# Kernel optimization log

Hardware: AMD Instinct MI355X
Metric: run time of the kernel (lower is better)

The kernel has to match this reference:

```python
import jax, jax.numpy as jnp
import numpy as np

B, S, D = 2, 512, 256

def setup_inputs() -> dict:
    key = jax.random.key(0)
    k1, k2, k3, k4, k5 = jax.random.split(key, 5)
    return {
        "query": jax.random.normal(k1, (B, S, D), dtype=jnp.float32),
        "key": jax.random.normal(k2, (B, S, D), dtype=jnp.float32),
        "value": jax.random.normal(k3, (B, S, D), dtype=jnp.float32),
        "Wm_w": jax.random.normal(k4, (D, D), dtype=jnp.float32) * (1.0 / np.sqrt(D)),
        "vm_w": jax.random.normal(k5, (1, D), dtype=jnp.float32) * (1.0 / np.sqrt(D)),
    }

def reference(query, key, value, Wm_w, vm_w):
    # pairwise difference: q.unsqueeze(1) - q.unsqueeze(2) -> [B, S, S, D]
    diff = query[:, None, :, :] - query[:, :, None, :]
    # Wm (Linear, no bias): [B,S,S,D] @ Wm_w^T, then tanh
    h = jnp.tanh(jnp.einsum('bijd,ed->bije', diff, Wm_w))
    # vm (Linear D->1, no bias) + squeeze -> scores [B, S, S]
    sjt = jnp.einsum('bije,e->bij', h, vm_w[0])
    # softmax over dim=2 (eval mode: dropout is identity)
    atten = jax.nn.softmax(sjt, axis=2)
    # bmm(atten, value) -> [B, S, D]
    context = jnp.einsum('bij,bjd->bid', atten, value)
    return context, atten
```

## Files before the change

kernel.cpp:

```cpp
#include <hip/hip_runtime.h>

#define B 2
#define S 512
#define D 256
#define C2L 2.885390081777927f
#define LOG2E 1.4426950408889634f

__global__ __launch_bounds__(256) void proj_kernel(const float* __restrict__ q,
                                                   const float* __restrict__ W,
                                                   float* __restrict__ EJ,
                                                   float* __restrict__ EN) {
    __shared__ float qlds[4 * D];
    const int t = threadIdx.x;
    const int b = blockIdx.x / (S / 4);
    const int i0 = (blockIdx.x % (S / 4)) * 4;
    const float* qbase = q + (size_t)(b * S + i0) * D;
    for (int idx = t; idx < 4 * D; idx += 256) qlds[idx] = qbase[idx];
    __syncthreads();
    const float* wr = W + (size_t)t * D;
    float a0 = 0.f, a1 = 0.f, a2 = 0.f, a3 = 0.f;
#pragma unroll 4
    for (int d = 0; d < D; ++d) {
        float w = wr[d];
        a0 = fmaf(qlds[d], w, a0);
        a1 = fmaf(qlds[D + d], w, a1);
        a2 = fmaf(qlds[2 * D + d], w, a2);
        a3 = fmaf(qlds[3 * D + d], w, a3);
    }
    a0 *= C2L; a1 *= C2L; a2 *= C2L; a3 *= C2L;
    float* ej = EJ + (size_t)(b * D + t) * S + i0;
    *(float4*)ej = make_float4(__builtin_amdgcn_exp2f(a0), __builtin_amdgcn_exp2f(a1),
                               __builtin_amdgcn_exp2f(a2), __builtin_amdgcn_exp2f(a3));
    EN[(size_t)(b * S + i0 + 0) * D + t] = __builtin_amdgcn_exp2f(-a0);
    EN[(size_t)(b * S + i0 + 1) * D + t] = __builtin_amdgcn_exp2f(-a1);
    EN[(size_t)(b * S + i0 + 2) * D + t] = __builtin_amdgcn_exp2f(-a2);
    EN[(size_t)(b * S + i0 + 3) * D + t] = __builtin_amdgcn_exp2f(-a3);
}

__global__ __launch_bounds__(512, 4) void score_kernel(const float* __restrict__ EJ,
                                                       const float* __restrict__ EN,
                                                       const float* __restrict__ vm,
                                                       float* __restrict__ sc) {
    __shared__ float fpair[2][128][2];
    __shared__ float wl[128];
    __shared__ float cred[8];

    const int t = threadIdx.x;
    const int bid = blockIdx.x;
    const int b = bid >> 8;
    const int m = bid & 255;
    const int eh = m & 1;
    const int mm = m >> 1;
    const int e0 = eh * 128;
    const int r0 = 2 * mm;
    const int q0 = 510 - 2 * mm;

    {
        const int rr = t >> 7, el = t & 127;
        const int row = ((rr < 2) ? r0 : q0) + (rr & 1);
        fpair[rr >> 1][el][rr & 1] = EN[((size_t)b * S + row) * D + e0 + el];
    }
    float pc = 0.f;
    if (t < 128) {
        float v = vm[e0 + t];
        wl[t] = -2.f * v;
        pc = v;
    }
#pragma unroll
    for (int off = 32; off; off >>= 1) pc += __shfl_xor(pc, off);
    if ((t & 63) == 0) cred[t >> 6] = pc;
    __syncthreads();
    float ch = 0.f;
#pragma unroll
    for (int wv = 0; wv < 8; ++wv) ch += cred[wv];

    const int segA = 511 - 2 * mm;
    const bool inA = t < segA;
    const int j = inA ? (r0 + 1 + t) : t;
    const int rb0 = inA ? r0 : q0;
    const float2* fp = (const float2*)&fpair[inA ? 0 : 1][0][0];
    const float* ejp = EJ + ((size_t)b * D + e0) * S + j;

    float a0 = 0.f, a1 = 0.f;
#pragma unroll 8
    for (int el = 0; el < 128; ++el) {
        float ev = ejp[(size_t)el * S];
        float2 f = fp[el];
        float w = wl[el];
        float y0 = fmaf(ev, f.x, 1.f);
        float y1 = fmaf(ev, f.y, 1.f);
        float rv = __builtin_amdgcn_rcpf(y0);
        float rn = __uint_as_float(0x7EF311C3u - __float_as_uint(y1));
        rn = rn * fmaf(-y1, rn, 2.f);
        rn = rn * fmaf(-y1, rn, 2.f);
        a0 = fmaf(w, rv, a0);
        a1 = fmaf(w, rn, a1);
    }

    float* sb = sc + ((size_t)eh * B + b) * S * S;
    sb[(size_t)rb0 * S + j] = a0;
    sb[(size_t)(rb0 + 1) * S + j] = a1;
    *(float2*)&sb[(size_t)j * S + rb0] =
        make_float2(fmaf(-2.f, ch, -a0), fmaf(-2.f, ch, -a1));
    if (t == 0) sb[(size_t)r0 * S + r0] = -ch;
    if (t == 1) sb[(size_t)q0 * S + q0] = -ch;
}

__global__ __launch_bounds__(512) void softctx_kernel(const float* __restrict__ sc,
                                                      const float* __restrict__ value,
                                                      float* __restrict__ att,
                                                      float* __restrict__ ctx) {
    __shared__ float a4[S][4];
    __shared__ float part[4][8][64][4];
    __shared__ float redm[4][2], reds[4][2];

    const int t = threadIdx.x;
    const int b = blockIdx.x >> 7;
    const int i0 = (blockIdx.x & 127) * 4;

    {
        const int row = t >> 7, jr = t & 127;
        const int lane = t & 63, half = (t >> 6) & 1;
        const float* s0r = sc + (size_t)(b * S + i0 + row) * S;
        const float* s1r = s0r + (size_t)B * S * S;
        float s0 = s0r[jr] + s1r[jr];
        float s1 = s0r[jr + 128] + s1r[jr + 128];
        float s2 = s0r[jr + 256] + s1r[jr + 256];
        float s3 = s0r[jr + 384] + s1r[jr + 384];
        float lm = fmaxf(fmaxf(s0, s1), fmaxf(s2, s3));
#pragma unroll
        for (int off = 32; off; off >>= 1) lm = fmaxf(lm, __shfl_xor(lm, off));
        if (lane == 0) redm[row][half] = lm;
        __syncthreads();
        float m = fmaxf(redm[row][0], redm[row][1]);
        float p0 = __builtin_amdgcn_exp2f((s0 - m) * LOG2E);
        float p1 = __builtin_amdgcn_exp2f((s1 - m) * LOG2E);
        float p2 = __builtin_amdgcn_exp2f((s2 - m) * LOG2E);
        float p3 = __builtin_amdgcn_exp2f((s3 - m) * LOG2E);
        float ls = (p0 + p1) + (p2 + p3);
#pragma unroll
        for (int off = 32; off; off >>= 1) ls += __shfl_xor(ls, off);
        if (lane == 0) reds[row][half] = ls;
        __syncthreads();
        float rinv = __builtin_amdgcn_rcpf(reds[row][0] + reds[row][1]);
        p0 *= rinv; p1 *= rinv; p2 *= rinv; p3 *= rinv;
        float* arow = att + (size_t)(b * S + i0 + row) * S;
        arow[jr] = p0; arow[jr + 128] = p1; arow[jr + 256] = p2; arow[jr + 384] = p3;
        a4[jr][row] = p0; a4[jr + 128][row] = p1;
        a4[jr + 256][row] = p2; a4[jr + 384][row] = p3;
    }
    __syncthreads();

    {
        const int dq = t & 63, js = t >> 6;
        float4 acc0 = {}, acc1 = {}, acc2 = {}, acc3 = {};
        const float* vb = value + (size_t)b * S * D + (size_t)dq * 4;
#pragma unroll 4
        for (int jj = 0; jj < 64; ++jj) {
            int j = js * 64 + jj;
            float4 v = *(const float4*)(vb + (size_t)j * D);
            float w0 = a4[j][0], w1 = a4[j][1], w2 = a4[j][2], w3 = a4[j][3];
            acc0.x = fmaf(w0, v.x, acc0.x); acc0.y = fmaf(w0, v.y, acc0.y);
            acc0.z = fmaf(w0, v.z, acc0.z); acc0.w = fmaf(w0, v.w, acc0.w);
            acc1.x = fmaf(w1, v.x, acc1.x); acc1.y = fmaf(w1, v.y, acc1.y);
            acc1.z = fmaf(w1, v.z, acc1.z); acc1.w = fmaf(w1, v.w, acc1.w);
            acc2.x = fmaf(w2, v.x, acc2.x); acc2.y = fmaf(w2, v.y, acc2.y);
            acc2.z = fmaf(w2, v.z, acc2.z); acc2.w = fmaf(w2, v.w, acc2.w);
            acc3.x = fmaf(w3, v.x, acc3.x); acc3.y = fmaf(w3, v.y, acc3.y);
            acc3.z = fmaf(w3, v.z, acc3.z); acc3.w = fmaf(w3, v.w, acc3.w);
        }
        *(float4*)&part[0][js][dq][0] = acc0;
        *(float4*)&part[1][js][dq][0] = acc1;
        *(float4*)&part[2][js][dq][0] = acc2;
        *(float4*)&part[3][js][dq][0] = acc3;
    }
    __syncthreads();
    if (t < 256) {
        const int row = t >> 6, dq = t & 63;
        float4 sum = {};
#pragma unroll
        for (int js = 0; js < 8; ++js) {
            float4 p = *(const float4*)&part[row][js][dq][0];
            sum.x += p.x; sum.y += p.y; sum.z += p.z; sum.w += p.w;
        }
        *(float4*)(ctx + (size_t)(b * S + i0 + row) * D + (size_t)dq * 4) = sum;
    }
}

extern "C" void kernel_launch(void* const* d_in, const int* in_sizes, int n_in,
                              void* d_out, int out_size, void* d_ws, size_t ws_size,
                              hipStream_t stream) {
    const float* q = (const float*)d_in[0];
    const float* value = (const float*)d_in[2];
    const float* W = (const float*)d_in[3];
    const float* vm = (const float*)d_in[4];

    float* ctx = (float*)d_out;
    float* att = ctx + (size_t)B * S * D;
    float* EJ = (float*)d_ws;
    float* EN = EJ + (size_t)B * D * S;
    float* SC = EN + (size_t)B * S * D;

    proj_kernel<<<B * (S / 4), 256, 0, stream>>>(q, W, EJ, EN);
    score_kernel<<<B * 256, 512, 0, stream>>>(EJ, EN, vm, SC);
    softctx_kernel<<<B * (S / 4), 512, 0, stream>>>(SC, value, att, ctx);
}
```

Before: 41.60 us.

## Fuse score computation into softmax-context kernel, dropping antisymmetry reuse

Merges the score kernel into the softmax/context kernel. Each block now computes full score rows for its 4 query rows directly from EJ/EN across all 256 features, then applies softmax and the value product. This removes the intermediate score buffer write/read and one kernel launch. In exchange it gives up the antisymmetric pair trick, which reused each computed score for the transposed entry, so score arithmetic roughly doubles.

Measured after the change: 48.43 us. 1.16x slower.

```diff
diff --git a/kernel.cpp b/kernel.cpp
--- a/kernel.cpp
+++ b/kernel.cpp
@@ -37,117 +37,85 @@
     EN[(size_t)(b * S + i0 + 3) * D + t] = __builtin_amdgcn_exp2f(-a3);
 }
 
-__global__ __launch_bounds__(512, 4) void score_kernel(const float* __restrict__ EJ,
-                                                       const float* __restrict__ EN,
-                                                       const float* __restrict__ vm,
-                                                       float* __restrict__ sc) {
-    __shared__ float fpair[2][128][2];
-    __shared__ float wl[128];
-    __shared__ float cred[8];
-
-    const int t = threadIdx.x;
-    const int bid = blockIdx.x;
-    const int b = bid >> 8;
-    const int m = bid & 255;
-    const int eh = m & 1;
-    const int mm = m >> 1;
-    const int e0 = eh * 128;
-    const int r0 = 2 * mm;
-    const int q0 = 510 - 2 * mm;
-
-    {
-        const int rr = t >> 7, el = t & 127;
-        const int row = ((rr < 2) ? r0 : q0) + (rr & 1);
-        fpair[rr >> 1][el][rr & 1] = EN[((size_t)b * S + row) * D + e0 + el];
-    }
-    float pc = 0.f;
-    if (t < 128) {
-        float v = vm[e0 + t];
-        wl[t] = -2.f * v;
-        pc = v;
-    }
-#pragma unroll
-    for (int off = 32; off; off >>= 1) pc += __shfl_xor(pc, off);
-    if ((t & 63) == 0) cred[t >> 6] = pc;
-    __syncthreads();
-    float ch = 0.f;
-#pragma unroll
-    for (int wv = 0; wv < 8; ++wv) ch += cred[wv];
-
-    const int segA = 511 - 2 * mm;
-    const bool inA = t < segA;
-    const int j = inA ? (r0 + 1 + t) : t;
-    const int rb0 = inA ? r0 : q0;
-    const float2* fp = (const float2*)&fpair[inA ? 0 : 1][0][0];
-    const float* ejp = EJ + ((size_t)b * D + e0) * S + j;
-
-    float a0 = 0.f, a1 = 0.f;
-#pragma unroll 8
-    for (int el = 0; el < 128; ++el) {
-        float ev = ejp[(size_t)el * S];
-        float2 f = fp[el];
-        float w = wl[el];
-        float y0 = fmaf(ev, f.x, 1.f);
-        float y1 = fmaf(ev, f.y, 1.f);
-        float rv = __builtin_amdgcn_rcpf(y0);
-        float rn = __uint_as_float(0x7EF311C3u - __float_as_uint(y1));
-        rn = rn * fmaf(-y1, rn, 2.f);
-        rn = rn * fmaf(-y1, rn, 2.f);
-        a0 = fmaf(w, rv, a0);
-        a1 = fmaf(w, rn, a1);
-    }
-
-    float* sb = sc + ((size_t)eh * B + b) * S * S;
-    sb[(size_t)rb0 * S + j] = a0;
-    sb[(size_t)(rb0 + 1) * S + j] = a1;
-    *(float2*)&sb[(size_t)j * S + rb0] =
-        make_float2(fmaf(-2.f, ch, -a0), fmaf(-2.f, ch, -a1));
-    if (t == 0) sb[(size_t)r0 * S + r0] = -ch;
-    if (t == 1) sb[(size_t)q0 * S + q0] = -ch;
-}
-
-__global__ __launch_bounds__(512) void softctx_kernel(const float* __restrict__ sc,
-                                                      const float* __restrict__ value,
-                                                      float* __restrict__ att,
-                                                      float* __restrict__ ctx) {
+__global__ __launch_bounds__(512) void fused_kernel(const float* __restrict__ EJ,
+                                                    const float* __restrict__ EN,
+                                                    const float* __restrict__ vm,
+                                                    const float* __restrict__ value,
+                                                    float* __restrict__ att,
+                                                    float* __restrict__ ctx) {
+    __shared__ float en4[D][4];
+    __shared__ float wl[D];
     __shared__ float a4[S][4];
     __shared__ float part[4][8][64][4];
-    __shared__ float redm[4][2], reds[4][2];
+    __shared__ float redm[4][8], reds[4][8];
 
     const int t = threadIdx.x;
     const int b = blockIdx.x >> 7;
     const int i0 = (blockIdx.x & 127) * 4;
 
+    if (t < D) wl[t] = -2.f * vm[t];
     {
-        const int row = t >> 7, jr = t & 127;
-        const int lane = t & 63, half = (t >> 6) & 1;
-        const float* s0r = sc + (size_t)(b * S + i0 + row) * S;
-        const float* s1r = s0r + (size_t)B * S * S;
-        float s0 = s0r[jr] + s1r[jr];
-        float s1 = s0r[jr + 128] + s1r[jr + 128];
-        float s2 = s0r[jr + 256] + s1r[jr + 256];
-        float s3 = s0r[jr + 384] + s1r[jr + 384];
-        float lm = fmaxf(fmaxf(s0, s1), fmaxf(s2, s3));
+        const int e = t & 255, r2 = (t >> 8) * 2;
+        en4[e][r2]     = EN[((size_t)(b * S + i0 + r2)) * D + e];
+        en4[e][r2 + 1] = EN[((size_t)(b * S + i0 + r2 + 1)) * D + e];
+    }
+    __syncthreads();
+
+    float acc[4] = {};
+    const float* ejp = EJ + (size_t)b * D * S + t;
+#pragma unroll 8
+    for (int e = 0; e < D; ++e) {
+        float ev = ejp[(size_t)e * S];
+        float w = wl[e];
+        float4 f = *(const float4*)&en4[e][0];
+        float y0 = fmaf(ev, f.x, 1.f);
+        float y1 = fmaf(ev, f.y, 1.f);
+        float y2 = fmaf(ev, f.z, 1.f);
+        float y3 = fmaf(ev, f.w, 1.f);
+        float r0 = __builtin_amdgcn_rcpf(y0);
+        float r2v = __builtin_amdgcn_rcpf(y2);
+        float r1 = __uint_as_float(0x7EF311C3u - __float_as_uint(y1));
+        r1 = r1 * fmaf(-y1, r1, 2.f);
+        r1 = r1 * fmaf(-y1, r1, 2.f);
+        float r3 = __uint_as_float(0x7EF311C3u - __float_as_uint(y3));
+        r3 = r3 * fmaf(-y3, r3, 2.f);
+        r3 = r3 * fmaf(-y3, r3, 2.f);
+        acc[0] = fmaf(w, r0, acc[0]);
+        acc[1] = fmaf(w, r1, acc[1]);
+        acc[2] = fmaf(w, r2v, acc[2]);
+        acc[3] = fmaf(w, r3, acc[3]);
+    }
+
+    const int lane = t & 63, wv = t >> 6;
+#pragma unroll
+    for (int r = 0; r < 4; ++r) {
+        float lm = acc[r];
 #pragma unroll
         for (int off = 32; off; off >>= 1) lm = fmaxf(lm, __shfl_xor(lm, off));
-        if (lane == 0) redm[row][half] = lm;
-        __syncthreads();
-        float m = fmaxf(redm[row][0], redm[row][1]);
-        float p0 = __builtin_amdgcn_exp2f((s0 - m) * LOG2E);
-        float p1 = __builtin_amdgcn_exp2f((s1 - m) * LOG2E);
-        float p2 = __builtin_amdgcn_exp2f((s2 - m) * LOG2E);
-        float p3 = __builtin_amdgcn_exp2f((s3 - m) * LOG2E);
-        float ls = (p0 + p1) + (p2 + p3);
+        if (lane == 0) redm[r][wv] = lm;
+    }
+    __syncthreads();
+    float p[4];
+#pragma unroll
+    for (int r = 0; r < 4; ++r) {
+        float m = redm[r][0];
+#pragma unroll
+        for (int w = 1; w < 8; ++w) m = fmaxf(m, redm[r][w]);
+        p[r] = __builtin_amdgcn_exp2f((acc[r] - m) * LOG2E);
+        float ls = p[r];
 #pragma unroll
         for (int off = 32; off; off >>= 1) ls += __shfl_xor(ls, off);
-        if (lane == 0) reds[row][half] = ls;
-        __syncthreads();
-        float rinv = __builtin_amdgcn_rcpf(reds[row][0] + reds[row][1]);
-        p0 *= rinv; p1 *= rinv; p2 *= rinv; p3 *= rinv;
-        float* arow = att + (size_t)(b * S + i0 + row) * S;
-        arow[jr] = p0; arow[jr + 128] = p1; arow[jr + 256] = p2; arow[jr + 384] = p3;
-        a4[jr][row] = p0; a4[jr + 128][row] = p1;
-        a4[jr + 256][row] = p2; a4[jr + 384][row] = p3;
+        if (lane == 0) reds[r][wv] = ls;
+    }
+    __syncthreads();
+#pragma unroll
+    for (int r = 0; r < 4; ++r) {
+        float s = 0.f;
+#pragma unroll
+        for (int w = 0; w < 8; ++w) s += reds[r][w];
+        float a = p[r] * __builtin_amdgcn_rcpf(s);
+        a4[t][r] = a;
+        att[(size_t)(b * S + i0 + r) * S + t] = a;
     }
     __syncthreads();
 
@@ -180,8 +148,8 @@
         float4 sum = {};
 #pragma unroll
         for (int js = 0; js < 8; ++js) {
-            float4 p = *(const float4*)&part[row][js][dq][0];
-            sum.x += p.x; sum.y += p.y; sum.z += p.z; sum.w += p.w;
+            float4 pt = *(const float4*)&part[row][js][dq][0];
+            sum.x += pt.x; sum.y += pt.y; sum.z += pt.z; sum.w += pt.w;
         }
         *(float4*)(ctx + (size_t)(b * S + i0 + row) * D + (size_t)dq * 4) = sum;
     }
@@ -199,9 +167,7 @@
     float* att = ctx + (size_t)B * S * D;
     float* EJ = (float*)d_ws;
     float* EN = EJ + (size_t)B * D * S;
-    float* SC = EN + (size_t)B * S * D;
 
     proj_kernel<<<B * (S / 4), 256, 0, stream>>>(q, W, EJ, EN);
-    score_kernel<<<B * 256, 512, 0, stream>>>(EJ, EN, vm, SC);
-    softctx_kernel<<<B * (S / 4), 512, 0, stream>>>(SC, value, att, ctx);
+    fused_kernel<<<B * (S / 4), 512, 0, stream>>>(EJ, EN, vm, value, att, ctx);
 }
```
